# Optimization experiments

Measured on AMD Instinct MI355X. Metric: run time of the kernel, lower is better.

## Reference

```python
import jax, jax.numpy as jnp
import numpy as np

V, E, M, Q, K_ANS, L = 100000, 300, 256, 64, 1024, 64
T = K_ANS * L
WINDOW_SIZES = (1, 2, 3, 4, 5)


def setup_inputs() -> dict:
    key = jax.random.key(0)
    ks = jax.random.split(key, 16)
    s = 0.05
    inp = {
        "data_q": jax.random.randint(ks[0], (Q,), 0, V, dtype=jnp.int32),
        "data_as_word": jax.random.randint(ks[1], (T,), 0, V, dtype=jnp.int32),
        "sizes": jnp.full((K_ANS,), L, dtype=jnp.int32),
        "emb": jax.random.normal(ks[2], (V, E), jnp.float32) * s,
        "W1": jax.random.normal(ks[3], (E, M), jnp.float32) * s,
        "b1": jnp.zeros((M,), jnp.float32),
        "W2": jax.random.normal(ks[4], (E, M), jnp.float32) * s,
        "b2": jnp.zeros((M,), jnp.float32),
        "Wl": jax.random.normal(ks[5], (len(WINDOW_SIZES) * M, M), jnp.float32) * s,
        "bl": jnp.zeros((M,), jnp.float32),
        "Ws": jax.random.normal(ks[6], (M, 1), jnp.float32) * s,
        "bs": jnp.zeros((1,), jnp.float32),
    }
    for i, w in enumerate(WINDOW_SIZES):
        inp[f"Wc{i+1}"] = jax.random.normal(ks[7 + i], (M, M, w), jnp.float32) * s
        inp[f"bc{i+1}"] = jnp.zeros((M,), jnp.float32)
    return inp


def _dmax(c, sizes, w):
    # Dynamic max pool: c is [Lc, M] conv+relu over the concatenated answer axis;
    # each answer k owns conv positions [start_k, start_k + sizes_k - w + 1).
    starts = jnp.concatenate([jnp.zeros((1,), sizes.dtype), jnp.cumsum(sizes)[:-1]])
    pos = jnp.arange(c.shape[0])
    seg = jnp.searchsorted(starts, pos, side="right") - 1  # answer id per position
    valid = pos < starts[seg] + sizes[seg] - (w - 1)
    vals = jnp.where(valid[:, None], c, -jnp.inf)
    return jax.ops.segment_max(vals, seg, num_segments=sizes.shape[0])  # [K, M]


def reference(data_q, data_as_word, sizes, emb, W1, b1, W2, b2,
              Wc1, bc1, Wc2, bc2, Wc3, bc3, Wc4, bc4, Wc5, bc5, Wl, bl, Ws, bs):
    # Gated projection layer: sigmoid(Wx) * tanh(Wx)
    proj = lambda x: jax.nn.sigmoid(x @ W1 + b1) * jnp.tanh(x @ W2 + b2)
    q_p = proj(emb[data_q])        # [Q, M]
    a_p = proj(emb[data_as_word])  # [T, M]
    # Attention: mm -> softmax over dim 0 of attention.T -> mm (as in original)
    att = q_p @ a_p.T                       # [Q, T]
    w_att = jax.nn.softmax(att.T, axis=0)   # [T, Q]
    ctx = w_att @ q_p                       # [T, M]
    sim = a_p * ctx                         # compare step ('mul')  [T, M]
    # Conv + dynamic max pooling per window size
    x = sim.T[None]                         # [1, M, T]
    convs = ((Wc1, bc1), (Wc2, bc2), (Wc3, bc3), (Wc4, bc4), (Wc5, bc5))
    pools = []
    for wsz, (Wc, bc) in zip(WINDOW_SIZES, convs):
        c = jax.lax.conv_general_dilated(
            x, Wc, (1,), "VALID", dimension_numbers=("NCH", "OIH", "NCH"))[0].T  # [T-w+1, M]
        c = jax.nn.relu(c + bc)
        pools.append(_dmax(c, sizes, wsz))  # [K, M]
    h = jnp.tanh(jnp.concatenate(pools, axis=1) @ Wl + bl)  # [K, M]
    logits = (h @ Ws + bs).reshape(-1)                       # [K]
    return jax.nn.log_softmax(logits, axis=0)
```

## Files before the change

### kernel.cpp

```cpp
#include <hip/hip_runtime.h>

typedef unsigned short u16;
typedef unsigned int u32;
using s16x8 = __attribute__((ext_vector_type(8))) short;
using f32x4 = __attribute__((ext_vector_type(4))) float;
using u16x4 = __attribute__((ext_vector_type(4))) u16;

#define DEV __device__ __forceinline__

DEV u16 f2bf(float f) {
    u32 u = __builtin_bit_cast(u32, f);
    u32 r = (u + 0x7FFFu + ((u >> 16) & 1u)) >> 16;
    return (u16)r;
}
DEV float bf2f(u16 h) { return __builtin_bit_cast(float, ((u32)h) << 16); }

DEV f32x4 mfma16(s16x8 a, s16x8 b, f32x4 c) {
    return __builtin_amdgcn_mfma_f32_16x16x32_bf16(a, b, c, 0, 0, 0);
}

#define GLOAD(g, l) __builtin_amdgcn_global_load_lds( \
    (const __attribute__((address_space(1))) unsigned int*)(g), \
    (__attribute__((address_space(3))) unsigned int*)(l), 16, 0, 0)

__global__ void k_prep(const float* W1, const float* W2, const float* Wl,
                       const float* Wc1, const float* Wc2, const float* Wc3,
                       const float* Wc4, const float* Wc5,
                       u16* WpT, u16* WlT, u16* WcT) {
    int idx = blockIdx.x * 256 + threadIdx.x;
    if (idx < 512 * 320) {
        int n = idx / 320, k = idx - n * 320;
        float v = 0.f;
        if (k < 300) v = (n < 256) ? W1[k * 256 + n] : W2[k * 256 + (n - 256)];
        WpT[idx] = f2bf(v);
    } else if (idx < 512 * 320 + 256 * 1280) {
        int j2 = idx - 512 * 320;
        int m = j2 / 1280, j = j2 - m * 1280;
        WlT[j2] = f2bf(Wl[j * 256 + m]);
    } else {
        int j3 = idx - (512 * 320 + 256 * 1280);
        if (j3 < 983040) {
            int wsz; int off;
            if (j3 < 65536)       { wsz = 1; off = 0; }
            else if (j3 < 196608) { wsz = 2; off = 65536; }
            else if (j3 < 393216) { wsz = 3; off = 196608; }
            else if (j3 < 655360) { wsz = 4; off = 393216; }
            else                  { wsz = 5; off = 655360; }
            int loc = j3 - off;
            int o = loc / (256 * wsz);
            int kk = loc - o * (256 * wsz);
            int dw = kk >> 8, i = kk & 255;
            const float* W = (wsz == 1) ? Wc1 : (wsz == 2) ? Wc2 : (wsz == 3) ? Wc3
                             : (wsz == 4) ? Wc4 : Wc5;
            WcT[j3] = f2bf(W[(o * 256 + i) * wsz + dw]);
        }
    }
}

__global__ void k_starts(const int* sizes, int* starts) {
    __shared__ int s[1024];
    int t = threadIdx.x;
    int v = sizes[t];
    s[t] = v;
    __syncthreads();
    for (int off = 1; off < 1024; off <<= 1) {
        int add = (t >= off) ? s[t - off] : 0;
        __syncthreads();
        s[t] += add;
        __syncthreads();
    }
    starts[t] = s[t] - v;
}

__global__ void k_qpt(const u16* qp, u16* qpT) {
    __shared__ u16 L[64 * 260];
    int tid = threadIdx.x;
    for (int j = tid; j < 2048; j += 256) {
        int q = j >> 5, c8 = (j & 31) * 8;
        *(s16x8*)(L + q * 260 + c8) = *(const s16x8*)(qp + q * 256 + c8);
    }
    __syncthreads();
    int m = tid;
    u16 buf[64];
#pragma unroll
    for (int q = 0; q < 64; ++q) buf[q] = L[q * 260 + m];
#pragma unroll
    for (int h = 0; h < 8; ++h)
        *(s16x8*)(qpT + m * 64 + h * 8) = *(const s16x8*)(buf + h * 8);
}

__launch_bounds__(512)
__global__ void k_proj(const int* idx, const float* emb, const u16* WpT,
                       const float* b1, const float* b2, u16* out) {
    __shared__ u16 X[64 * 320];
    int tid = threadIdx.x;
    long row0 = (long)blockIdx.x * 64;
    {
        int r = tid >> 3, part = tid & 7;
        const float* src = emb + (long)idx[row0 + r] * 300;
        char* xrow = (char*)X + r * 640;
        u32 swz = (u32)((r & 7) << 4);
        for (int c0 = part * 40; c0 < part * 40 + 40; c0 += 4) {
            float4 f;
            if (c0 + 4 <= 300) f = *(const float4*)(src + c0);
            else {
                f.x = (c0 < 300) ? src[c0] : 0.f;
                f.y = (c0 + 1 < 300) ? src[c0 + 1] : 0.f;
                f.z = (c0 + 2 < 300) ? src[c0 + 2] : 0.f;
                f.w = (c0 + 3 < 300) ? src[c0 + 3] : 0.f;
            }
            u16x4 h = { f2bf(f.x), f2bf(f.y), f2bf(f.z), f2bf(f.w) };
            *(u16x4*)(xrow + ((u32)(c0 * 2) ^ swz)) = h;
        }
    }
    __syncthreads();
    int wv = tid >> 6, lane = tid & 63, l15 = lane & 15, lq = lane >> 4;
    f32x4 acc[4][4] = {};
    for (int s = 0; s < 10; ++s) {
        s16x8 a[4], b[4];
#pragma unroll
        for (int c = 0; c < 4; ++c) {
            int mt = 2 * wv + (c & 1) + (c >> 1) * 16;
            int o = mt * 16 + l15;
            a[c] = *(const s16x8*)(WpT + o * 320 + s * 32 + lq * 8);
        }
#pragma unroll
        for (int nt = 0; nt < 4; ++nt) {
            int r = nt * 16 + l15;
            b[nt] = *(const s16x8*)((const char*)X + r * 640 +
                                    ((u32)(s * 64 + lq * 16) ^ ((u32)(r & 7) << 4)));
        }
#pragma unroll
        for (int c = 0; c < 4; ++c)
#pragma unroll
            for (int nt = 0; nt < 4; ++nt)
                acc[c][nt] = mfma16(a[c], b[nt], acc[c][nt]);
    }
    __syncthreads();
    u16* Y = X;
#pragma unroll
    for (int c = 0; c < 2; ++c) {
        int o0 = (2 * wv + c) * 16 + lq * 4;
#pragma unroll
        for (int nt = 0; nt < 4; ++nt) {
            int t = nt * 16 + l15;
#pragma unroll
            for (int r = 0; r < 4; ++r) {
                float xs = acc[c][nt][r] + b1[o0 + r];
                float xt = acc[c + 2][nt][r] + b2[o0 + r];
                float v = (1.f / (1.f + __expf(-xs))) * tanhf(xt);
                Y[t * 256 + o0 + r] = f2bf(v);
            }
        }
    }
    __syncthreads();
    for (int j = tid; j < 2048; j += 512) {
        int t = j >> 5, c8 = (j & 31) * 8;
        *(s16x8*)(out + (row0 + t) * 256 + c8) = *(const s16x8*)(Y + t * 256 + c8);
    }
}

__launch_bounds__(256)
__global__ void k_att(const u16* qp, const u16* ap, float* att,
                      float* partm, float* parts) {
    __shared__ float AT[64][68];
    __shared__ float Lm[4][64], Ls[4][64];
    int tid = threadIdx.x;
    long t0 = (long)blockIdx.x * 64;
    int wv = tid >> 6, lane = tid & 63, l15 = lane & 15, lq = lane >> 4;
    f32x4 acc[4] = {};
    const u16* brow = ap + (t0 + wv * 16 + l15) * 256 + lq * 8;
    const u16* arow = qp + l15 * 256 + lq * 8;
    for (int s = 0; s < 8; ++s) {
        s16x8 b = *(const s16x8*)(brow + s * 32);
#pragma unroll
        for (int mt = 0; mt < 4; ++mt) {
            s16x8 a = *(const s16x8*)(arow + mt * 16 * 256 + s * 32);
            acc[mt] = mfma16(a, b, acc[mt]);
        }
    }
    int t = wv * 16 + l15;
#pragma unroll
    for (int mt = 0; mt < 4; ++mt) {
        *(f32x4*)(att + (t0 + t) * 64 + mt * 16 + lq * 4) = acc[mt];
        *(f32x4*)&AT[t][mt * 16 + lq * 4] = acc[mt];
    }
    __syncthreads();
    {
        int q = tid & 63, sub = tid >> 6;
        float m = -3.0e38f, s = 0.f;
#pragma unroll
        for (int i = 0; i < 16; ++i) {
            float v = AT[sub * 16 + i][q];
            if (v > m) { s = s * __expf(m - v) + 1.f; m = v; }
            else s += __expf(v - m);
        }
        Lm[sub][q] = m; Ls[sub][q] = s;
    }
    __syncthreads();
    if (tid < 64) {
        int q = tid;
        float m = Lm[0][q], s = Ls[0][q];
#pragma unroll
        for (int i = 1; i < 4; ++i) {
            float m2 = Lm[i][q], s2 = Ls[i][q];
            float mn = fmaxf(m, m2);
            s = s * __expf(m - mn) + s2 * __expf(m2 - mn);
            m = mn;
        }
        partm[blockIdx.x * 64 + q] = m;
        parts[blockIdx.x * 64 + q] = s;
    }
}

__launch_bounds__(512)
__global__ void k_red2(const float* partm, const float* parts, float* mx, float* rden) {
    __shared__ float Lm[8][64], Ls[8][64];
    int q = threadIdx.x & 63, sub = threadIdx.x >> 6;
    float m = -3.0e38f, s = 0.f;
    for (int b = sub; b < 1024; b += 8) {
        float m2 = partm[b * 64 + q], s2 = parts[b * 64 + q];
        float mn = fmaxf(m, m2);
        s = s * __expf(m - mn) + s2 * __expf(m2 - mn);
        m = mn;
    }
    Lm[sub][q] = m; Ls[sub][q] = s;
    __syncthreads();
    if (sub == 0) {
#pragma unroll
        for (int i = 1; i < 8; ++i) {
            float m2 = Lm[i][q], s2 = Ls[i][q];
            float mn = fmaxf(m, m2);
            s = s * __expf(m - mn) + s2 * __expf(m2 - mn);
            m = mn;
        }
        mx[q] = m;
        rden[q] = 1.f / s;
    }
}

__launch_bounds__(256)
__global__ void k_ctx(const float* att, const float* mx, const float* rden,
                      const u16* qpT, const u16* ap, u16* sim) {
    __shared__ u16 Y[64 * 264];
    int tid = threadIdx.x;
    long t0 = (long)blockIdx.x * 64;
    int wv = tid >> 6, lane = tid & 63, l15 = lane & 15, lq = lane >> 4;
    f32x4 acc[16] = {};
#pragma unroll
    for (int s = 0; s < 2; ++s) {
        int q0 = s * 32 + lq * 8;
        const float* arow = att + (t0 + wv * 16 + l15) * 64 + q0;
        f32x4 v0 = *(const f32x4*)(arow);
        f32x4 v1 = *(const f32x4*)(arow + 4);
        f32x4 m0 = *(const f32x4*)(mx + q0);
        f32x4 m1 = *(const f32x4*)(mx + q0 + 4);
        f32x4 r0 = *(const f32x4*)(rden + q0);
        f32x4 r1 = *(const f32x4*)(rden + q0 + 4);
        s16x8 a;
#pragma unroll
        for (int e = 0; e < 4; ++e) {
            a[e]     = (short)f2bf(__expf(v0[e] - m0[e]) * r0[e]);
            a[e + 4] = (short)f2bf(__expf(v1[e] - m1[e]) * r1[e]);
        }
#pragma unroll
        for (int nt = 0; nt < 16; ++nt) {
            s16x8 b = *(const s16x8*)(qpT + (nt * 16 + l15) * 64 + q0);
            acc[nt] = mfma16(a, b, acc[nt]);
        }
    }
#pragma unroll
    for (int nt = 0; nt < 16; ++nt) {
        int m = nt * 16 + l15;
        int t = wv * 16 + lq * 4;
#pragma unroll
        for (int r = 0; r < 4; ++r) Y[(t + r) * 264 + m] = f2bf(acc[nt][r]);
    }
    __syncthreads();
    for (int j = tid; j < 2048; j += 256) {
        int t = j >> 5, c8 = (j & 31) * 8;
        s16x8 y = *(const s16x8*)(Y + t * 264 + c8);
        s16x8 a8 = *(const s16x8*)(ap + (t0 + t) * 256 + c8);
        s16x8 o;
#pragma unroll
        for (int e = 0; e < 8; ++e)
            o[e] = (short)f2bf(bf2f((u16)a8[e]) * bf2f((u16)y[e]));
        *(s16x8*)(sim + (t0 + t) * 256 + c8) = o;
    }
}

__launch_bounds__(512)
__global__ void k_conv(const u16* sim, const u16* WcT,
                       const int* starts, const int* sizes,
                       const float* bc1, const float* bc2, const float* bc3,
                       const float* bc4, const float* bc5,
                       u16* pools, int Ttot) {
    __shared__ u16 LB[2][32768];
    int tid = threadIdx.x;
    int wv = tid >> 6, lane = tid & 63, l15 = lane & 15, lq = lane >> 4;
    int wm = wv >> 2, wn = wv & 3;
    int b = blockIdx.x;
    long s0 = starts[4 * b];
    int row8 = lane >> 3, seg = lane & 7;
    u32 sA = ((u32)(seg * 16)) ^ (((u32)(row8 & 7)) << 4);

    auto STAGE = [&](int nb, int w_, int dw_, int ic_) {
        int Krow = 256 * w_;
        long wbase = 65536L * ((w_ * (w_ - 1)) / 2);
#pragma unroll
        for (int it = 0; it < 4; ++it) {
            int c = wv * 4 + it;
            long g = s0 + dw_ + c * 8 + row8;
            if (g >= Ttot) g = Ttot - 1;
            const char* srcA = (const char*)sim + g * 512 + ic_ * 128 + sA;
            GLOAD(srcA, (char*)LB[nb] + c * 1024);
        }
#pragma unroll
        for (int it = 0; it < 4; ++it) {
            int c = wv * 4 + it;
            int o = c * 8 + row8;
            const char* srcB = (const char*)WcT +
                2L * (wbase + (long)o * Krow + dw_ * 256 + ic_ * 64) + sA;
            GLOAD(srcB, (char*)LB[nb] + 32768 + c * 1024);
        }
    };
    auto ADV = [](int& w_, int& dw_, int& ic_) {
        if (++ic_ == 4) { ic_ = 0; if (++dw_ == w_) { dw_ = 0; ++w_; } }
    };

    int wS = 1, dwS = 0, icS = 0;
    STAGE(0, wS, dwS, icS);
    ADV(wS, dwS, icS);
    __syncthreads();

    int buf = 0;
    f32x4 acc[8][4] = {};
    int wC = 1, dwC = 0, icC = 0;
    for (int t = 0; t < 60; ++t) {
        if (t < 59) { STAGE(buf ^ 1, wS, dwS, icS); ADV(wS, dwS, icS); }
        const char* Ab = (const char*)LB[buf];
        const char* Bb = (const char*)LB[buf] + 32768;
#pragma unroll
        for (int ks = 0; ks < 2; ++ks) {
            s16x8 A8[8], B4[4];
#pragma unroll
            for (int mt = 0; mt < 8; ++mt) {
                int row = wm * 128 + mt * 16 + l15;
                A8[mt] = *(const s16x8*)(Ab + row * 128 +
                          (((u32)(ks * 64 + lq * 16)) ^ (((u32)(row & 7)) << 4)));
            }
#pragma unroll
            for (int nt = 0; nt < 4; ++nt) {
                int o = wn * 64 + nt * 16 + l15;
                B4[nt] = *(const s16x8*)(Bb + o * 128 +
                          (((u32)(ks * 64 + lq * 16)) ^ (((u32)(o & 7)) << 4)));
            }
            __builtin_amdgcn_s_setprio(1);
#pragma unroll
            for (int mt = 0; mt < 8; ++mt)
#pragma unroll
                for (int nt = 0; nt < 4; ++nt)
                    acc[mt][nt] = mfma16(A8[mt], B4[nt], acc[mt][nt]);
            __builtin_amdgcn_s_setprio(0);
        }
        if (++icC == 4) {
            icC = 0;
            if (++dwC == wC) {
                dwC = 0;
                const float* bc = (wC == 1) ? bc1 : (wC == 2) ? bc2 : (wC == 3) ? bc3
                                  : (wC == 4) ? bc4 : bc5;
#pragma unroll
                for (int a2 = 0; a2 < 2; ++a2) {
                    int kans = b * 4 + wm * 2 + a2;
                    int valid = sizes[kans] - wC + 1;
#pragma unroll
                    for (int nt = 0; nt < 4; ++nt) {
                        float m = -3.0e38f;
#pragma unroll
                        for (int mth = 0; mth < 4; ++mth) {
                            int mt = a2 * 4 + mth;
#pragma unroll
                            for (int r = 0; r < 4; ++r) {
                                int pp = mth * 16 + lq * 4 + r;
                                float v = (pp < valid) ? acc[mt][nt][r] : -3.0e38f;
                                m = fmaxf(m, v);
                            }
                        }
                        m = fmaxf(m, __shfl_xor(m, 16, 64));
                        m = fmaxf(m, __shfl_xor(m, 32, 64));
                        if (lq == 0) {
                            int o = wn * 64 + nt * 16 + l15;
                            float pool = fmaxf(m + bc[o], 0.f);
                            pools[(long)kans * 1280 + (wC - 1) * 256 + o] = f2bf(pool);
                        }
                    }
                }
#pragma unroll
                for (int mt = 0; mt < 8; ++mt)
#pragma unroll
                    for (int nt = 0; nt < 4; ++nt)
                        acc[mt][nt] = f32x4{0.f, 0.f, 0.f, 0.f};
                ++wC;
            }
        }
        __syncthreads();
        buf ^= 1;
    }
}

__launch_bounds__(256)
__global__ void k_head(const u16* pools, const u16* WlT,
                       const float* bl, const float* Ws, const float* bs,
                       float* logits) {
    int tid = threadIdx.x;
    int k0 = blockIdx.x * 64;
    int wv = tid >> 6, lane = tid & 63, l15 = lane & 15, lq = lane >> 4;
    f32x4 acc[4][4] = {};
    for (int s = 0; s < 40; ++s) {
        s16x8 a[4], b[4];
#pragma unroll
        for (int mt = 0; mt < 4; ++mt) {
            int m = (wv * 4 + mt) * 16 + l15;
            a[mt] = *(const s16x8*)(WlT + (long)m * 1280 + s * 32 + lq * 8);
        }
#pragma unroll
        for (int nt = 0; nt < 4; ++nt) {
            int kk = k0 + nt * 16 + l15;
            b[nt] = *(const s16x8*)(pools + (long)kk * 1280 + s * 32 + lq * 8);
        }
#pragma unroll
        for (int mt = 0; mt < 4; ++mt)
#pragma unroll
            for (int nt = 0; nt < 4; ++nt)
                acc[mt][nt] = mfma16(a[mt], b[nt], acc[mt][nt]);
    }
    __shared__ float PS[4][4][16];
#pragma unroll
    for (int nt = 0; nt < 4; ++nt) {
        float p = 0.f;
#pragma unroll
        for (int mt = 0; mt < 4; ++mt) {
            int m0 = (wv * 4 + mt) * 16 + lq * 4;
#pragma unroll
            for (int r = 0; r < 4; ++r) {
                float h = tanhf(acc[mt][nt][r] + bl[m0 + r]);
                p += h * Ws[m0 + r];
            }
        }
        p += __shfl_xor(p, 16, 64);
        p += __shfl_xor(p, 32, 64);
        if (lq == 0) PS[wv][nt][l15] = p;
    }
    __syncthreads();
    if (tid < 64) {
        int nt = tid >> 4, i = tid & 15;
        float v = PS[0][nt][i] + PS[1][nt][i] + PS[2][nt][i] + PS[3][nt][i] + bs[0];
        logits[k0 + nt * 16 + i] = v;
    }
}

__global__ void k_lsm(const float* logits, float* out) {
    __shared__ float r1[16], r2[16];
    int tid = threadIdx.x;
    float v = logits[tid];
    float m = v;
#pragma unroll
    for (int off = 32; off >= 1; off >>= 1) m = fmaxf(m, __shfl_xor(m, off, 64));
    if ((tid & 63) == 0) r1[tid >> 6] = m;
    __syncthreads();
    if (tid < 16) {
        float t = r1[tid];
#pragma unroll
        for (int off = 8; off >= 1; off >>= 1) t = fmaxf(t, __shfl_xor(t, off, 64));
        r1[tid] = t;
    }
    __syncthreads();
    m = r1[0];
    float e = __expf(v - m);
    float s = e;
#pragma unroll
    for (int off = 32; off >= 1; off >>= 1) s += __shfl_xor(s, off, 64);
    if ((tid & 63) == 0) r2[tid >> 6] = s;
    __syncthreads();
    if (tid < 16) {
        float t = r2[tid];
#pragma unroll
        for (int off = 8; off >= 1; off >>= 1) t += __shfl_xor(t, off, 64);
        r2[tid] = t;
    }
    __syncthreads();
    out[tid] = v - m - logf(r2[0]);
}

extern "C" void kernel_launch(void* const* d_in, const int* in_sizes, int n_in,
                              void* d_out, int out_size, void* d_ws, size_t ws_size,
                              hipStream_t stream) {
    const int*   data_q  = (const int*)d_in[0];
    const int*   data_as = (const int*)d_in[1];
    const int*   sizes   = (const int*)d_in[2];
    const float* emb = (const float*)d_in[3];
    const float* W1  = (const float*)d_in[4];
    const float* b1  = (const float*)d_in[5];
    const float* W2  = (const float*)d_in[6];
    const float* b2  = (const float*)d_in[7];
    const float* Wl  = (const float*)d_in[8];
    const float* bl  = (const float*)d_in[9];
    const float* Ws  = (const float*)d_in[10];
    const float* bs  = (const float*)d_in[11];
    const float* Wc1 = (const float*)d_in[12]; const float* bc1 = (const float*)d_in[13];
    const float* Wc2 = (const float*)d_in[14]; const float* bc2 = (const float*)d_in[15];
    const float* Wc3 = (const float*)d_in[16]; const float* bc3 = (const float*)d_in[17];
    const float* Wc4 = (const float*)d_in[18]; const float* bc4 = (const float*)d_in[19];
    const float* Wc5 = (const float*)d_in[20]; const float* bc5 = (const float*)d_in[21];
    int Ttot = in_sizes[1];

    char* ws = (char*)d_ws;
    u16*   WpT    = (u16*)  (ws + 0);
    u16*   WlT    = (u16*)  (ws + 327680);
    u16*   WcT    = (u16*)  (ws + 983040);
    u16*   qp     = (u16*)  (ws + 2949120);
    u16*   ap     = (u16*)  (ws + 2981888);
    float* att    = (float*)(ws + 36536320);
    float* mx     = (float*)(ws + 53379072);
    float* rden   = (float*)(ws + 53379328);
    u16*   sim    = (u16*)  (ws + 53379584);
    u16*   pools  = (u16*)  (ws + 86934016);
    float* logits = (float*)(ws + 89555456);
    int*   starts = (int*)  (ws + 89559552);
    u16*   qpT    = (u16*)  (ws + 89563648);
    float* partm  = (float*)pools;
    float* parts  = (float*)((char*)pools + 262144);

    k_prep<<<5760, 256, 0, stream>>>(W1, W2, Wl, Wc1, Wc2, Wc3, Wc4, Wc5, WpT, WlT, WcT);
    k_starts<<<1, 1024, 0, stream>>>(sizes, starts);
    k_proj<<<1024, 512, 0, stream>>>(data_as, emb, WpT, b1, b2, ap);
    k_proj<<<1, 512, 0, stream>>>(data_q, emb, WpT, b1, b2, qp);
    k_qpt<<<1, 256, 0, stream>>>(qp, qpT);
    k_att<<<1024, 256, 0, stream>>>(qp, ap, att, partm, parts);
    k_red2<<<1, 512, 0, stream>>>(partm, parts, mx, rden);
    k_ctx<<<1024, 256, 0, stream>>>(att, mx, rden, qpT, ap, sim);
    k_conv<<<256, 512, 0, stream>>>(sim, WcT, starts, sizes, bc1, bc2, bc3, bc4, bc5,
                                    pools, Ttot);
    k_head<<<16, 256, 0, stream>>>(pools, WlT, bl, Ws, bs, logits);
    k_lsm<<<1, 1024, 0, stream>>>(logits, (float*)d_out);
}
```

Measured before the change: 369.0 us.

## Split softmax reduction out of attention kernel, stage tiles in swizzled LDS, fold starts scan

```diff
diff --git a/kernel.cpp b/kernel.cpp
--- a/kernel.cpp
+++ b/kernel.cpp
@@ -26,8 +26,30 @@
 __global__ void k_prep(const float* W1, const float* W2, const float* Wl,
                        const float* Wc1, const float* Wc2, const float* Wc3,
                        const float* Wc4, const float* Wc5,
-                       u16* WpT, u16* WlT, u16* WcT) {
-    int idx = blockIdx.x * 256 + threadIdx.x;
+                       u16* WpT, u16* WlT, u16* WcT,
+                       const int* sizes, int* starts) {
+    int tid = threadIdx.x;
+    if (blockIdx.x == 5760) {
+        __shared__ int ps[256];
+        int t4 = tid * 4;
+        int v0 = sizes[t4], v1 = sizes[t4 + 1], v2 = sizes[t4 + 2], v3 = sizes[t4 + 3];
+        int sum = v0 + v1 + v2 + v3;
+        ps[tid] = sum;
+        __syncthreads();
+        for (int off = 1; off < 256; off <<= 1) {
+            int add = (tid >= off) ? ps[tid - off] : 0;
+            __syncthreads();
+            ps[tid] += add;
+            __syncthreads();
+        }
+        int base = tid ? ps[tid - 1] : 0;
+        starts[t4] = base;
+        starts[t4 + 1] = base + v0;
+        starts[t4 + 2] = base + v0 + v1;
+        starts[t4 + 3] = base + v0 + v1 + v2;
+        return;
+    }
+    int idx = blockIdx.x * 256 + tid;
     if (idx < 512 * 320) {
         int n = idx / 320, k = idx - n * 320;
         float v = 0.f;
@@ -57,21 +79,6 @@
     }
 }
 
-__global__ void k_starts(const int* sizes, int* starts) {
-    __shared__ int s[1024];
-    int t = threadIdx.x;
-    int v = sizes[t];
-    s[t] = v;
-    __syncthreads();
-    for (int off = 1; off < 1024; off <<= 1) {
-        int add = (t >= off) ? s[t - off] : 0;
-        __syncthreads();
-        s[t] += add;
-        __syncthreads();
-    }
-    starts[t] = s[t] - v;
-}
-
 __global__ void k_qpt(const u16* qp, u16* qpT) {
     __shared__ u16 L[64 * 260];
     int tid = threadIdx.x;
@@ -161,47 +168,53 @@
 }
 
 __launch_bounds__(256)
-__global__ void k_att(const u16* qp, const u16* ap, float* att,
-                      float* partm, float* parts) {
-    __shared__ float AT[64][68];
-    __shared__ float Lm[4][64], Ls[4][64];
+__global__ void k_att(const u16* qp, const u16* ap, float* att) {
+    __shared__ u16 Q[64 * 256];
+    __shared__ u16 A[64 * 256];
     int tid = threadIdx.x;
     long t0 = (long)blockIdx.x * 64;
+    for (int j = tid; j < 2048; j += 256) {
+        int r = j >> 5, c8 = (j & 31) * 8;
+        u32 dst = (u32)(c8 * 2) ^ ((u32)(r & 7) << 4);
+        *(s16x8*)((char*)Q + r * 512 + dst) = *(const s16x8*)(qp + r * 256 + c8);
+        *(s16x8*)((char*)A + r * 512 + dst) = *(const s16x8*)(ap + (t0 + r) * 256 + c8);
+    }
+    __syncthreads();
     int wv = tid >> 6, lane = tid & 63, l15 = lane & 15, lq = lane >> 4;
     f32x4 acc[4] = {};
-    const u16* brow = ap + (t0 + wv * 16 + l15) * 256 + lq * 8;
-    const u16* arow = qp + l15 * 256 + lq * 8;
     for (int s = 0; s < 8; ++s) {
-        s16x8 b = *(const s16x8*)(brow + s * 32);
+        int brow = wv * 16 + l15;
+        s16x8 b = *(const s16x8*)((const char*)A + brow * 512 +
+                                  ((u32)(s * 64 + lq * 16) ^ ((u32)(brow & 7) << 4)));
 #pragma unroll
         for (int mt = 0; mt < 4; ++mt) {
-            s16x8 a = *(const s16x8*)(arow + mt * 16 * 256 + s * 32);
+            int arow = mt * 16 + l15;
+            s16x8 a = *(const s16x8*)((const char*)Q + arow * 512 +
+                                      ((u32)(s * 64 + lq * 16) ^ ((u32)(arow & 7) << 4)));
             acc[mt] = mfma16(a, b, acc[mt]);
         }
     }
-    int t = wv * 16 + l15;
 #pragma unroll
     for (int mt = 0; mt < 4; ++mt) {
-        *(f32x4*)(att + (t0 + t) * 64 + mt * 16 + lq * 4) = acc[mt];
-        *(f32x4*)&AT[t][mt * 16 + lq * 4] = acc[mt];
-    }
-    __syncthreads();
-    {
-        int q = tid & 63, sub = tid >> 6;
-        float m = -3.0e38f, s = 0.f;
-#pragma unroll
-        for (int i = 0; i < 16; ++i) {
-            float v = AT[sub * 16 + i][q];
-            if (v > m) { s = s * __expf(m - v) + 1.f; m = v; }
-            else s += __expf(v - m);
-        }
-        Lm[sub][q] = m; Ls[sub][q] = s;
-    }
-    __syncthreads();
-    if (tid < 64) {
-        int q = tid;
-        float m = Lm[0][q], s = Ls[0][q];
-#pragma unroll
+        long t = t0 + wv * 16 + l15;
+        *(f32x4*)(att + t * 64 + mt * 16 + lq * 4) = acc[mt];
+    }
+}
+
+__global__ void k_red1(const float* att, float* partm, float* parts) {
+    int tid = threadIdx.x;
+    int q = tid & 63, sub = tid >> 6;
+    long t0 = (long)blockIdx.x * 512;
+    float m = -3.0e38f, s = 0.f;
+    for (int i = sub; i < 512; i += 4) {
+        float v = att[(t0 + i) * 64 + q];
+        if (v > m) { s = s * __expf(m - v) + 1.f; m = v; }
+        else s += __expf(v - m);
+    }
+    __shared__ float Lm[4][64], Ls[4][64];
+    Lm[sub][q] = m; Ls[sub][q] = s;
+    __syncthreads();
+    if (sub == 0) {
         for (int i = 1; i < 4; ++i) {
             float m2 = Lm[i][q], s2 = Ls[i][q];
             float mn = fmaxf(m, m2);
@@ -213,30 +226,17 @@
     }
 }
 
-__launch_bounds__(512)
 __global__ void k_red2(const float* partm, const float* parts, float* mx, float* rden) {
-    __shared__ float Lm[8][64], Ls[8][64];
-    int q = threadIdx.x & 63, sub = threadIdx.x >> 6;
+    int q = threadIdx.x;
     float m = -3.0e38f, s = 0.f;
-    for (int b = sub; b < 1024; b += 8) {
+    for (int b = 0; b < 128; ++b) {
         float m2 = partm[b * 64 + q], s2 = parts[b * 64 + q];
         float mn = fmaxf(m, m2);
         s = s * __expf(m - mn) + s2 * __expf(m2 - mn);
         m = mn;
     }
-    Lm[sub][q] = m; Ls[sub][q] = s;
-    __syncthreads();
-    if (sub == 0) {
-#pragma unroll
-        for (int i = 1; i < 8; ++i) {
-            float m2 = Lm[i][q], s2 = Ls[i][q];
-            float mn = fmaxf(m, m2);
-            s = s * __expf(m - mn) + s2 * __expf(m2 - mn);
-            m = mn;
-        }
-        mx[q] = m;
-        rden[q] = 1.f / s;
-    }
+    mx[q] = m;
+    rden[q] = 1.f / s;
 }
 
 __launch_bounds__(256)
@@ -531,13 +531,14 @@
     float* partm  = (float*)pools;
     float* parts  = (float*)((char*)pools + 262144);
 
-    k_prep<<<5760, 256, 0, stream>>>(W1, W2, Wl, Wc1, Wc2, Wc3, Wc4, Wc5, WpT, WlT, WcT);
-    k_starts<<<1, 1024, 0, stream>>>(sizes, starts);
+    k_prep<<<5761, 256, 0, stream>>>(W1, W2, Wl, Wc1, Wc2, Wc3, Wc4, Wc5,
+                                     WpT, WlT, WcT, sizes, starts);
     k_proj<<<1024, 512, 0, stream>>>(data_as, emb, WpT, b1, b2, ap);
     k_proj<<<1, 512, 0, stream>>>(data_q, emb, WpT, b1, b2, qp);
     k_qpt<<<1, 256, 0, stream>>>(qp, qpT);
-    k_att<<<1024, 256, 0, stream>>>(qp, ap, att, partm, parts);
-    k_red2<<<1, 512, 0, stream>>>(partm, parts, mx, rden);
+    k_att<<<1024, 256, 0, stream>>>(qp, ap, att);
+    k_red1<<<128, 256, 0, stream>>>(att, partm, parts);
+    k_red2<<<1, 64, 0, stream>>>(partm, parts, mx, rden);
     k_ctx<<<1024, 256, 0, stream>>>(att, mx, rden, qpT, ap, sim);
     k_conv<<<256, 512, 0, stream>>>(sim, WcT, starts, sizes, bc1, bc2, bc3, bc4, bc5,
                                     pools, Ttot);
```

Result: no change. 361.9 us (-1.9%).
